# Performance work log

Measured on AMD Instinct MI355X. Metric: run time of the kernel, lower is better.

The kernel has to match this reference:

```python
import jax, jax.numpy as jnp
import numpy as np
import math

B, S, C = 4, 2048, 128
H, DK, DV, K = 8, 64, 64, 3


def setup_inputs() -> dict:
    key = jax.random.key(0)
    ks = jax.random.split(key, 12)
    sd = 0.05
    return {
        "x": jax.random.normal(ks[0], (B, S, C), dtype=jnp.float32),
        "length": jax.random.randint(ks[1], (B,), 1, S + 1, dtype=jnp.int32),
        "wq": jax.random.normal(ks[2], (H * DK, C, K), dtype=jnp.float32) * sd,
        "bq": jnp.zeros((H * DK,), dtype=jnp.float32),
        "wk": jax.random.normal(ks[3], (H * DK, C, K), dtype=jnp.float32) * sd,
        "bk": jnp.zeros((H * DK,), dtype=jnp.float32),
        "wv": jax.random.normal(ks[4], (H * DV, C), dtype=jnp.float32) * sd,
        "bv": jnp.zeros((H * DV,), dtype=jnp.float32),
        "w1": jax.random.normal(ks[5], (DV, H * DV), dtype=jnp.float32) * sd,
        "b1": jnp.zeros((DV,), dtype=jnp.float32),
        "w2": jax.random.normal(ks[6], (1, DV), dtype=jnp.float32) * sd,
        "b2": jnp.zeros((1,), dtype=jnp.float32),
    }


def _causal_conv(x, w, b):
    # x: (b,s,c), w: (o,c,k) torch Conv1d layout -> (b,s,o), causal (left) padding
    y = jax.lax.conv_general_dilated(
        x.transpose(0, 2, 1), w, window_strides=(1,), padding=[(K - 1, 0)],
        dimension_numbers=("NCH", "OIH", "NCH"))
    return y.transpose(0, 2, 1) + b


def _split_heads(x, d):
    b, s, _ = x.shape
    return x.reshape(b, s, H, d).transpose(0, 2, 1, 3)  # (b,h,s,d)


def reference(x, length, wq, bq, wk, bk, wv, bv, w1, b1, w2, b2):
    q = _split_heads(_causal_conv(x, wq, bq), DK)            # (b,h,s,dk)
    k = _split_heads(_causal_conv(x, wk, bk), DK)            # (b,h,s,dk)
    v = _split_heads(jax.nn.relu(x @ wv.T + bv), DV)         # (b,h,s,dv)

    attn = jnp.einsum("bhqd,bhkd->bhqk", q, k) / math.sqrt(DK)
    # future mask: additive -1e9 above the diagonal (matches triu * -1e9 + softmax)
    future = jnp.triu(jnp.ones((S, S), dtype=attn.dtype), k=1) * (-1e9)
    score = jax.nn.softmax(attn + future, axis=-1)
    # padding mask: zero query rows >= length[b]
    row_valid = (jnp.arange(S)[None, :] < length[:, None]).astype(score.dtype)
    score = score * row_valid[:, None, :, None]              # (b,h,s,s)

    out1 = jnp.einsum("bhqk,bhkd->bhqd", score, v)           # (b,h,s,dv)
    out2 = out1.transpose(0, 2, 1, 3).reshape(x.shape[0], S, H * DV)
    out3 = jax.nn.relu(out2 @ w1.T + b1) @ w2.T + b2         # (b,s,1)
    return out3, score
```

## Files before the change

### kernel.cpp

```cpp
#include <hip/hip_runtime.h>

#define S_ 2048
#define C_ 128
#define B_ 4
#define H_ 8
#define D_ 64

typedef __attribute__((ext_vector_type(8))) short bf16x8;
typedef __attribute__((ext_vector_type(4))) float f32x4;

__device__ inline unsigned short f2bf(float f) {
    union { float f; unsigned int u; } c; c.f = f;
    unsigned int u = c.u;
    unsigned int r = (u + 0x7FFFu + ((u >> 16) & 1u)) >> 16;
    return (unsigned short)r;
}
__device__ inline float bf2f(unsigned short s) {
    union { unsigned int u; float f; } c; c.u = ((unsigned int)s) << 16;
    return c.f;
}

__global__ __launch_bounds__(256) void prep_kernel(
    const float* __restrict__ x,
    const float* __restrict__ wq, const float* __restrict__ wk,
    const float* __restrict__ wv, const float* __restrict__ w1,
    unsigned short* __restrict__ xh,
    unsigned short* __restrict__ wPackQ, unsigned short* __restrict__ wPackK,
    unsigned short* __restrict__ wPackV, float* __restrict__ w1T4)
{
    int idx = blockIdx.x * 256 + threadIdx.x;
    if (idx < 262144) {
        float4 v = *(const float4*)&x[idx * 4];
        ushort4 o;
        o.x = f2bf(v.x); o.y = f2bf(v.y); o.z = f2bf(v.z); o.w = f2bf(v.w);
        *(ushort4*)&xh[idx * 4] = o;
    } else if (idx < 458752) {
        int i = idx - 262144;
        int t = i >> 16, r = i & 65535;
        int o = r >> 7, c = r & 127;
        wPackQ[i] = f2bf(wq[o * 384 + c * 3 + t]);
    } else if (idx < 655360) {
        int i = idx - 458752;
        int t = i >> 16, r = i & 65535;
        int o = r >> 7, c = r & 127;
        wPackK[i] = f2bf(wk[o * 384 + c * 3 + t]);
    } else if (idx < 720896) {
        int i = idx - 655360;
        wPackV[i] = f2bf(wv[i]);
    } else if (idx < 753664) {
        int i = idx - 720896;
        int jj = i & 3, d = (i >> 2) & 63, jb = i >> 8;
        w1T4[i] = w1[d * 512 + jb * 4 + jj];
    }
}

__global__ __launch_bounds__(256) void qkv_kernel(
    const unsigned short* __restrict__ xh,
    const unsigned short* __restrict__ wPackQ, const unsigned short* __restrict__ wPackK,
    const unsigned short* __restrict__ wPackV,
    const float* __restrict__ bq, const float* __restrict__ bk,
    const float* __restrict__ bv,
    unsigned short* __restrict__ Qh, unsigned short* __restrict__ Kh,
    unsigned short* __restrict__ VhT)
{
    __shared__ __align__(16) short xs[130 * 136];
    __shared__ __align__(16) short ws[64 * 136];

    int s0 = blockIdx.x * 128;
    int h = blockIdx.y;
    int b = blockIdx.z;
    int bh = b * H_ + h;
    int tid = threadIdx.x;
    int w = tid >> 6;
    int lane = tid & 63;
    int col = lane & 15;
    int quad = lane >> 4;

    for (int i = tid; i < 2080; i += 256) {
        int row = i >> 4, c8 = (i & 15) << 3;
        int s = s0 - 2 + row;
        uint4 v = {0u, 0u, 0u, 0u};
        if (s >= 0) v = *(const uint4*)&xh[((long)b * S_ + s) * C_ + c8];
        *(uint4*)&xs[row * 136 + c8] = v;
    }

    for (int sec = 0; sec < 3; sec++) {
        const unsigned short* wsel = (sec == 0) ? wPackQ : (sec == 1) ? wPackK : wPackV;
        int tlo = (sec == 2) ? 2 : 0;

        f32x4 acc[2][4];
        #pragma unroll
        for (int rt = 0; rt < 2; rt++)
            #pragma unroll
            for (int nt = 0; nt < 4; nt++) acc[rt][nt] = (f32x4){0.f, 0.f, 0.f, 0.f};

        for (int t = tlo; t < 3; t++) {
            if (!(sec == 0 && t == 0)) __syncthreads();
            long wbase = (sec == 2) ? ((long)h * 8192)
                                    : ((long)t * 65536 + (long)h * 8192);
            for (int i = tid; i < 1024; i += 256) {
                int row = i >> 4, c8 = (i & 15) << 3;
                *(uint4*)&ws[row * 136 + c8] = *(const uint4*)&wsel[wbase + row * 128 + c8];
            }
            __syncthreads();

            #pragma unroll
            for (int kc = 0; kc < 4; kc++) {
                int ko = kc * 32 + quad * 8;
                bf16x8 a0 = *(const bf16x8*)&xs[(w * 32 + col + t) * 136 + ko];
                bf16x8 a1 = *(const bf16x8*)&xs[(w * 32 + 16 + col + t) * 136 + ko];
                #pragma unroll
                for (int nt = 0; nt < 4; nt++) {
                    bf16x8 bfr = *(const bf16x8*)&ws[(nt * 16 + col) * 136 + ko];
                    acc[0][nt] = __builtin_amdgcn_mfma_f32_16x16x32_bf16(a0, bfr, acc[0][nt], 0, 0, 0);
                    acc[1][nt] = __builtin_amdgcn_mfma_f32_16x16x32_bf16(a1, bfr, acc[1][nt], 0, 0, 0);
                }
            }
        }

        if (sec == 0) {
            #pragma unroll
            for (int nt = 0; nt < 4; nt++) {
                float bias = bq[h * 64 + nt * 16 + col];
                #pragma unroll
                for (int rt = 0; rt < 2; rt++)
                    #pragma unroll
                    for (int r = 0; r < 4; r++) {
                        int s = s0 + w * 32 + rt * 16 + quad * 4 + r;
                        Qh[((long)bh * S_ + s) * D_ + nt * 16 + col] =
                            f2bf((acc[rt][nt][r] + bias) * 0.18033688011112042f);
                    }
            }
        } else if (sec == 1) {
            #pragma unroll
            for (int nt = 0; nt < 4; nt++) {
                float bias = bk[h * 64 + nt * 16 + col];
                #pragma unroll
                for (int rt = 0; rt < 2; rt++)
                    #pragma unroll
                    for (int r = 0; r < 4; r++) {
                        int s = s0 + w * 32 + rt * 16 + quad * 4 + r;
                        Kh[((long)bh * S_ + s) * D_ + nt * 16 + col] =
                            f2bf(acc[rt][nt][r] + bias);
                    }
            }
        } else {
            __syncthreads();
            #pragma unroll
            for (int nt = 0; nt < 4; nt++) {
                float bias = bv[h * 64 + nt * 16 + col];
                #pragma unroll
                for (int rt = 0; rt < 2; rt++)
                    #pragma unroll
                    for (int r = 0; r < 4; r++) {
                        int sl = w * 32 + rt * 16 + quad * 4 + r;
                        ws[(nt * 16 + col) * 136 + sl] =
                            (short)f2bf(fmaxf(acc[rt][nt][r] + bias, 0.f));
                    }
            }
            __syncthreads();
            for (int i = tid; i < 1024; i += 256) {
                int row = i >> 4, c8 = (i & 15) << 3;
                *(uint4*)&VhT[((long)bh * D_ + row) * S_ + s0 + c8] =
                    *(const uint4*)&ws[row * 136 + c8];
            }
        }
    }
}

#define PST 78
__global__ __launch_bounds__(256) void attn_kernel(
    const unsigned short* __restrict__ Qh, const unsigned short* __restrict__ Kh,
    const unsigned short* __restrict__ VhT, const int* __restrict__ length,
    float* __restrict__ score, float* __restrict__ out2)
{
    __shared__ __align__(16) short Kbuf[2][2][64 * 72];
    __shared__ __align__(16) short Pfh[64 * PST];

    int idx = blockIdx.x;
    int xcd = idx & 7;
    int slot = idx >> 3;
    int t = slot >> 2;
    int qt = (t < 16) ? t : 47 - t;
    int bh = xcd * 4 + (slot & 3);
    int b = bh >> 3, h = bh & 7;
    int q0 = qt * 64;
    int tid = threadIdx.x;
    int w = tid >> 6;
    int lane = tid & 63;
    int col = lane & 15;
    int quad = lane >> 4;
    int len = length[b];

    const unsigned short* Qb = Qh + (long)bh * S_ * D_;
    const unsigned short* Kb = Kh + (long)bh * S_ * D_;
    const unsigned short* Vtb = VhT + (long)bh * D_ * S_;
    float* scb = score + (long)bh * S_ * S_;

    if (q0 >= len) {
        f32x4 z = (f32x4){0.f, 0.f, 0.f, 0.f};
        for (int kt2 = 0; kt2 < 32; kt2++) {
            #pragma unroll
            for (int it = 0; it < 4; it++) {
                int idx2 = tid + it * 256;
                int rr = idx2 >> 4, cc = idx2 & 15;
                __builtin_nontemporal_store(z,
                    (f32x4*)&scb[(long)(q0 + rr) * S_ + kt2 * 64 + cc * 4]);
            }
        }
        #pragma unroll
        for (int it = 0; it < 4; it++) {
            int idx2 = tid + it * 256;
            int rr = idx2 >> 4, cc = idx2 & 15;
            *(f32x4*)&out2[((long)(b * S_ + q0 + rr)) * 512 + h * 64 + cc * 4] = z;
        }
        return;
    }

    int srow_ = tid >> 2, sc16_ = (tid & 3) * 16;

    int arow = w * 16 + col;
    bf16x8 aq0 = *(const bf16x8*)&Qb[(q0 + arow) * D_ + quad * 8];
    bf16x8 aq1 = *(const bf16x8*)&Qb[(q0 + arow) * D_ + 32 + quad * 8];

    float lrun[4];
    #pragma unroll
    for (int r = 0; r < 4; r++) lrun[r] = 0.f;

    {
        *(uint4*)&Kbuf[0][0][srow_ * 72 + sc16_]     = *(const uint4*)&Kb[srow_ * D_ + sc16_];
        *(uint4*)&Kbuf[0][0][srow_ * 72 + sc16_ + 8] = *(const uint4*)&Kb[srow_ * D_ + sc16_ + 8];
    }
    __syncthreads();

    for (int kt = 0; kt <= qt; kt++) {
        int buf = kt & 1;
        if (kt < qt) {
            *(uint4*)&Kbuf[1 - buf][0][srow_ * 72 + sc16_] =
                *(const uint4*)&Kb[((kt + 1) * 64 + srow_) * D_ + sc16_];
            *(uint4*)&Kbuf[1 - buf][0][srow_ * 72 + sc16_ + 8] =
                *(const uint4*)&Kb[((kt + 1) * 64 + srow_) * D_ + sc16_ + 8];
        }

        f32x4 acc[4];
        #pragma unroll
        for (int n = 0; n < 4; n++) acc[n] = (f32x4){0.f, 0.f, 0.f, 0.f};
        #pragma unroll
        for (int n = 0; n < 4; n++) {
            bf16x8 b0 = *(const bf16x8*)&Kbuf[buf][0][(n * 16 + col) * 72 + quad * 8];
            acc[n] = __builtin_amdgcn_mfma_f32_16x16x32_bf16(aq0, b0, acc[n], 0, 0, 0);
            bf16x8 b1 = *(const bf16x8*)&Kbuf[buf][0][(n * 16 + col) * 72 + 32 + quad * 8];
            acc[n] = __builtin_amdgcn_mfma_f32_16x16x32_bf16(aq1, b1, acc[n], 0, 0, 0);
        }
        if (kt == qt) {
            #pragma unroll
            for (int n = 0; n < 4; n++) {
                int kk = kt * 64 + n * 16 + col;
                #pragma unroll
                for (int r = 0; r < 4; r++) {
                    int q = q0 + w * 16 + quad * 4 + r;
                    if (kk > q) acc[n][r] = -1.0e30f;
                }
            }
        }
        #pragma unroll
        for (int r = 0; r < 4; r++) {
            lrun[r] += exp2f(acc[0][r]) + exp2f(acc[1][r]) +
                       exp2f(acc[2][r]) + exp2f(acc[3][r]);
        }
        __syncthreads();
    }

    #pragma unroll
    for (int off = 1; off < 16; off <<= 1) {
        #pragma unroll
        for (int r = 0; r < 4; r++) lrun[r] += __shfl_xor(lrun[r], off, 64);
    }
    float linv[4];
    #pragma unroll
    for (int r = 0; r < 4; r++) linv[r] = 1.0f / lrun[r];

    f32x4 oacc[4];
    #pragma unroll
    for (int n = 0; n < 4; n++) oacc[n] = (f32x4){0.f, 0.f, 0.f, 0.f};

    int prow = w * 16 + quad * 4;
    int rlo = lane >> 4;
    int c4 = (lane & 15) * 4;

#define STAGE2(HALF, KT) do { \
    *(uint4*)&Kbuf[HALF][0][srow_ * 72 + sc16_] = \
        *(const uint4*)&Kb[((KT) * 64 + srow_) * D_ + sc16_]; \
    *(uint4*)&Kbuf[HALF][0][srow_ * 72 + sc16_ + 8] = \
        *(const uint4*)&Kb[((KT) * 64 + srow_) * D_ + sc16_ + 8]; \
    *(uint4*)&Kbuf[HALF][1][srow_ * 72 + sc16_] = \
        *(const uint4*)&Vtb[srow_ * S_ + (KT) * 64 + sc16_]; \
    *(uint4*)&Kbuf[HALF][1][srow_ * 72 + sc16_ + 8] = \
        *(const uint4*)&Vtb[srow_ * S_ + (KT) * 64 + sc16_ + 8]; \
} while (0)

#define TILE2(HALF, KT) do { \
    f32x4 acc[4]; \
    _Pragma("unroll") \
    for (int n = 0; n < 4; n++) acc[n] = (f32x4){0.f, 0.f, 0.f, 0.f}; \
    _Pragma("unroll") \
    for (int n = 0; n < 4; n++) { \
        bf16x8 b0 = *(const bf16x8*)&Kbuf[HALF][0][(n * 16 + col) * 72 + quad * 8]; \
        acc[n] = __builtin_amdgcn_mfma_f32_16x16x32_bf16(aq0, b0, acc[n], 0, 0, 0); \
        bf16x8 b1 = *(const bf16x8*)&Kbuf[HALF][0][(n * 16 + col) * 72 + 32 + quad * 8]; \
        acc[n] = __builtin_amdgcn_mfma_f32_16x16x32_bf16(aq1, b1, acc[n], 0, 0, 0); \
    } \
    bool diag = ((KT) == qt); \
    _Pragma("unroll") \
    for (int n = 0; n < 4; n++) { \
        int kk = (KT) * 64 + n * 16 + col; \
        _Pragma("unroll") \
        for (int r = 0; r < 4; r++) { \
            int q = q0 + prow + r; \
            float pv = exp2f(acc[n][r]) * linv[r]; \
            if (q >= len || (diag && kk > q)) pv = 0.f; \
            Pfh[(prow + r) * PST + n * 16 + col] = (short)f2bf(pv); \
        } \
    } \
    bf16x8 pa0 = *(const bf16x8*)&Pfh[(w * 16 + col) * PST + quad * 8]; \
    bf16x8 pa1 = *(const bf16x8*)&Pfh[(w * 16 + col) * PST + 32 + quad * 8]; \
    _Pragma("unroll") \
    for (int n = 0; n < 4; n++) { \
        bf16x8 vv0 = *(const bf16x8*)&Kbuf[HALF][1][(n * 16 + col) * 72 + quad * 8]; \
        oacc[n] = __builtin_amdgcn_mfma_f32_16x16x32_bf16(pa0, vv0, oacc[n], 0, 0, 0); \
        bf16x8 vv1 = *(const bf16x8*)&Kbuf[HALF][1][(n * 16 + col) * 72 + 32 + quad * 8]; \
        oacc[n] = __builtin_amdgcn_mfma_f32_16x16x32_bf16(pa1, vv1, oacc[n], 0, 0, 0); \
    } \
    _Pragma("unroll") \
    for (int j = 0; j < 4; j++) { \
        int row = w * 16 + j * 4 + rlo; \
        uint2 pk = *(const uint2*)&Pfh[row * PST + c4]; \
        f32x4 v; \
        v[0] = bf2f((unsigned short)(pk.x & 0xFFFFu)); \
        v[1] = bf2f((unsigned short)(pk.x >> 16)); \
        v[2] = bf2f((unsigned short)(pk.y & 0xFFFFu)); \
        v[3] = bf2f((unsigned short)(pk.y >> 16)); \
        __builtin_nontemporal_store(v, \
            (f32x4*)&scb[(long)(q0 + row) * S_ + (KT) * 64 + c4]); \
    } \
} while (0)

    STAGE2(0, 0);
    __syncthreads();
    {
        int kt = 0;
        while (true) {
            if (kt < qt) STAGE2(1, kt + 1);
            TILE2(0, kt);
            __syncthreads();
            kt++; if (kt > qt) break;
            if (kt < qt) STAGE2(0, kt + 1);
            TILE2(1, kt);
            __syncthreads();
            kt++; if (kt > qt) break;
        }
    }
#undef STAGE2
#undef TILE2

    #pragma unroll
    for (int n = 0; n < 4; n++) {
        #pragma unroll
        for (int r = 0; r < 4; r++) {
            int q = q0 + w * 16 + quad * 4 + r;
            out2[((long)(b * S_ + q)) * 512 + h * 64 + n * 16 + col] = oacc[n][r];
        }
    }

    f32x4 z = (f32x4){0.f, 0.f, 0.f, 0.f};
    for (int kt2 = qt + 1; kt2 < 32; kt2++) {
        #pragma unroll
        for (int it = 0; it < 4; it++) {
            int idx2 = tid + it * 256;
            int rr = idx2 >> 4, cc = idx2 & 15;
            __builtin_nontemporal_store(z,
                (f32x4*)&scb[(long)(q0 + rr) * S_ + kt2 * 64 + cc * 4]);
        }
    }
}

__global__ __launch_bounds__(256) void mlp_kernel(
    const float* __restrict__ out2, const float* __restrict__ w1T4,
    const float* __restrict__ b1, const float* __restrict__ w2,
    const float* __restrict__ b2, float* __restrict__ out3)
{
    __shared__ __align__(16) float xr[2048];
    int sg0 = blockIdx.x * 4;
    int tid = threadIdx.x;
    for (int i = tid; i < 512; i += 256)
        *(f32x4*)&xr[i * 4] = *(const f32x4*)&out2[(long)sg0 * 512 + i * 4];
    __syncthreads();

    int sl = tid >> 6, d = tid & 63;
    float acc = 0.f;
    #pragma unroll 4
    for (int jb = 0; jb < 128; jb++) {
        f32x4 xv = *(const f32x4*)&xr[sl * 512 + jb * 4];
        f32x4 wv = *(const f32x4*)&w1T4[jb * 256 + d * 4];
        acc += xv[0] * wv[0] + xv[1] * wv[1] + xv[2] * wv[2] + xv[3] * wv[3];
    }
    float hval = fmaxf(acc + b1[d], 0.f);
    float p = hval * w2[d];
    #pragma unroll
    for (int off = 32; off > 0; off >>= 1) p += __shfl_xor(p, off, 64);
    if (d == 0) out3[sg0 + sl] = p + b2[0];
}

extern "C" void kernel_launch(void* const* d_in, const int* in_sizes, int n_in,
                              void* d_out, int out_size, void* d_ws, size_t ws_size,
                              hipStream_t stream) {
    const float* x      = (const float*)d_in[0];
    const int*   length = (const int*)  d_in[1];
    const float* wq     = (const float*)d_in[2];
    const float* bq     = (const float*)d_in[3];
    const float* wk     = (const float*)d_in[4];
    const float* bk     = (const float*)d_in[5];
    const float* wv     = (const float*)d_in[6];
    const float* bv     = (const float*)d_in[7];
    const float* w1     = (const float*)d_in[8];
    const float* b1     = (const float*)d_in[9];
    const float* w2     = (const float*)d_in[10];
    const float* b2     = (const float*)d_in[11];

    float* out3  = (float*)d_out;
    float* score = (float*)d_out + 8192;

    float* ws  = (float*)d_ws;
    unsigned short* xh     = (unsigned short*)ws;  ws += 524288;
    unsigned short* wPackQ = (unsigned short*)ws;  ws += 98304;
    unsigned short* wPackK = (unsigned short*)ws;  ws += 98304;
    unsigned short* wPackV = (unsigned short*)ws;  ws += 32768;
    float* w1T4 = ws;  ws += 32768;
    unsigned short* Qh  = (unsigned short*)ws;  ws += 2097152;
    unsigned short* Kh  = (unsigned short*)ws;  ws += 2097152;
    unsigned short* VhT = (unsigned short*)ws;  ws += 2097152;
    float* o2  = ws;  ws += 4194304;

    hipLaunchKernelGGL(prep_kernel, dim3(2944), dim3(256), 0, stream,
                       x, wq, wk, wv, w1, xh, wPackQ, wPackK, wPackV, w1T4);
    hipLaunchKernelGGL(qkv_kernel, dim3(16, 8, 4), dim3(256), 0, stream,
                       xh, wPackQ, wPackK, wPackV, bq, bk, bv, Qh, Kh, VhT);
    hipLaunchKernelGGL(attn_kernel, dim3(1024), dim3(256), 0, stream,
                       Qh, Kh, VhT, length, score, o2);
    hipLaunchKernelGGL(mlp_kernel, dim3(2048), dim3(256), 0, stream,
                       o2, w1T4, b1, w2, b2, out3);
}
```

Measured before the change: 634.3 us.

## Split softmax row-sum pass into separate split-K kernel with atomic accumulation

Moves the first pass of the two-pass softmax (row sums of exp scores) out of the attention kernel into a new lsum_kernel. That kernel splits the causal key range into chunks of four tiles across many blocks and combines partial sums with atomicAdd into a buffer zeroed in the prep kernel. The attention kernel then only loads reciprocal sums and runs the second pass. The aim is to remove the serial, load-imbalanced first pass and expose more parallelism. The cost is an extra launch, K reads straight from global memory without LDS staging, and atomic traffic.

```diff
diff --git a/kernel.cpp b/kernel.cpp
--- a/kernel.cpp
+++ b/kernel.cpp
@@ -26,7 +26,8 @@
     const float* __restrict__ wv, const float* __restrict__ w1,
     unsigned short* __restrict__ xh,
     unsigned short* __restrict__ wPackQ, unsigned short* __restrict__ wPackK,
-    unsigned short* __restrict__ wPackV, float* __restrict__ w1T4)
+    unsigned short* __restrict__ wPackV, float* __restrict__ w1T4,
+    float* __restrict__ lbuf)
 {
     int idx = blockIdx.x * 256 + threadIdx.x;
     if (idx < 262144) {
@@ -51,6 +52,8 @@
         int i = idx - 720896;
         int jj = i & 3, d = (i >> 2) & 63, jb = i >> 8;
         w1T4[i] = w1[d * 512 + jb * 4 + jj];
+    } else if (idx < 819200) {
+        lbuf[idx - 753664] = 0.f;
     }
 }
 
@@ -168,10 +171,81 @@
     }
 }
 
+__global__ __launch_bounds__(256) void lsum_kernel(
+    const unsigned short* __restrict__ Qh, const unsigned short* __restrict__ Kh,
+    const int* __restrict__ length, float* __restrict__ lbuf)
+{
+    int qt = blockIdx.x;
+    int bh = blockIdx.y;
+    int ck = blockIdx.z;
+    int kt0 = ck * 4;
+    if (kt0 > qt) return;
+    int b = bh >> 3;
+    int len = length[b];
+    int q0 = qt * 64;
+    if (q0 >= len) return;
+
+    int tid = threadIdx.x;
+    int w = tid >> 6, lane = tid & 63, col = lane & 15, quad = lane >> 4;
+    const unsigned short* Qb = Qh + (long)bh * S_ * D_;
+    const unsigned short* Kb = Kh + (long)bh * S_ * D_;
+
+    int arow = w * 16 + col;
+    bf16x8 aq0 = *(const bf16x8*)&Qb[(q0 + arow) * D_ + quad * 8];
+    bf16x8 aq1 = *(const bf16x8*)&Qb[(q0 + arow) * D_ + 32 + quad * 8];
+
+    float lrun[4];
+    #pragma unroll
+    for (int r = 0; r < 4; r++) lrun[r] = 0.f;
+
+    int ktend = (kt0 + 3 < qt) ? kt0 + 3 : qt;
+    for (int kt = kt0; kt <= ktend; kt++) {
+        f32x4 acc[4];
+        #pragma unroll
+        for (int n = 0; n < 4; n++) acc[n] = (f32x4){0.f, 0.f, 0.f, 0.f};
+        #pragma unroll
+        for (int n = 0; n < 4; n++) {
+            const unsigned short* kp = &Kb[(kt * 64 + n * 16 + col) * D_ + quad * 8];
+            bf16x8 kf0 = *(const bf16x8*)kp;
+            bf16x8 kf1 = *(const bf16x8*)(kp + 32);
+            acc[n] = __builtin_amdgcn_mfma_f32_16x16x32_bf16(aq0, kf0, acc[n], 0, 0, 0);
+            acc[n] = __builtin_amdgcn_mfma_f32_16x16x32_bf16(aq1, kf1, acc[n], 0, 0, 0);
+        }
+        if (kt == qt) {
+            #pragma unroll
+            for (int n = 0; n < 4; n++) {
+                int kk = kt * 64 + n * 16 + col;
+                #pragma unroll
+                for (int r = 0; r < 4; r++) {
+                    int q = q0 + w * 16 + quad * 4 + r;
+                    if (kk > q) acc[n][r] = -1.0e30f;
+                }
+            }
+        }
+        #pragma unroll
+        for (int r = 0; r < 4; r++) {
+            lrun[r] += exp2f(acc[0][r]) + exp2f(acc[1][r]) +
+                       exp2f(acc[2][r]) + exp2f(acc[3][r]);
+        }
+    }
+
+    #pragma unroll
+    for (int off = 1; off < 16; off <<= 1) {
+        #pragma unroll
+        for (int r = 0; r < 4; r++) lrun[r] += __shfl_xor(lrun[r], off, 64);
+    }
+    if (col == 0) {
+        #pragma unroll
+        for (int r = 0; r < 4; r++)
+            atomicAdd(&lbuf[bh * S_ + q0 + w * 16 + quad * 4 + r], lrun[r]);
+    }
+}
+
 #define PST 78
 __global__ __launch_bounds__(256) void attn_kernel(
     const unsigned short* __restrict__ Qh, const unsigned short* __restrict__ Kh,
     const unsigned short* __restrict__ VhT, const int* __restrict__ length,
+    const float* __restrict__ lbuf,
     float* __restrict__ score, float* __restrict__ out2)
 {
     __shared__ __align__(16) short Kbuf[2][2][64 * 72];
@@ -223,62 +297,12 @@
     bf16x8 aq0 = *(const bf16x8*)&Qb[(q0 + arow) * D_ + quad * 8];
     bf16x8 aq1 = *(const bf16x8*)&Qb[(q0 + arow) * D_ + 32 + quad * 8];
 
-    float lrun[4];
-    #pragma unroll
-    for (int r = 0; r < 4; r++) lrun[r] = 0.f;
-
+    float linv[4];
     {
-        *(uint4*)&Kbuf[0][0][srow_ * 72 + sc16_]     = *(const uint4*)&Kb[srow_ * D_ + sc16_];
-        *(uint4*)&Kbuf[0][0][srow_ * 72 + sc16_ + 8] = *(const uint4*)&Kb[srow_ * D_ + sc16_ + 8];
-    }
-    __syncthreads();
-
-    for (int kt = 0; kt <= qt; kt++) {
-        int buf = kt & 1;
-        if (kt < qt) {
-            *(uint4*)&Kbuf[1 - buf][0][srow_ * 72 + sc16_] =
-                *(const uint4*)&Kb[((kt + 1) * 64 + srow_) * D_ + sc16_];
-            *(uint4*)&Kbuf[1 - buf][0][srow_ * 72 + sc16_ + 8] =
-                *(const uint4*)&Kb[((kt + 1) * 64 + srow_) * D_ + sc16_ + 8];
-        }
-
-        f32x4 acc[4];
-        #pragma unroll
-        for (int n = 0; n < 4; n++) acc[n] = (f32x4){0.f, 0.f, 0.f, 0.f};
-        #pragma unroll
-        for (int n = 0; n < 4; n++) {
-            bf16x8 b0 = *(const bf16x8*)&Kbuf[buf][0][(n * 16 + col) * 72 + quad * 8];
-            acc[n] = __builtin_amdgcn_mfma_f32_16x16x32_bf16(aq0, b0, acc[n], 0, 0, 0);
-            bf16x8 b1 = *(const bf16x8*)&Kbuf[buf][0][(n * 16 + col) * 72 + 32 + quad * 8];
-            acc[n] = __builtin_amdgcn_mfma_f32_16x16x32_bf16(aq1, b1, acc[n], 0, 0, 0);
-        }
-        if (kt == qt) {
-            #pragma unroll
-            for (int n = 0; n < 4; n++) {
-                int kk = kt * 64 + n * 16 + col;
-                #pragma unroll
-                for (int r = 0; r < 4; r++) {
-                    int q = q0 + w * 16 + quad * 4 + r;
-                    if (kk > q) acc[n][r] = -1.0e30f;
-                }
-            }
-        }
-        #pragma unroll
-        for (int r = 0; r < 4; r++) {
-            lrun[r] += exp2f(acc[0][r]) + exp2f(acc[1][r]) +
-                       exp2f(acc[2][r]) + exp2f(acc[3][r]);
-        }
-        __syncthreads();
-    }
-
-    #pragma unroll
-    for (int off = 1; off < 16; off <<= 1) {
-        #pragma unroll
-        for (int r = 0; r < 4; r++) lrun[r] += __shfl_xor(lrun[r], off, 64);
-    }
-    float linv[4];
-    #pragma unroll
-    for (int r = 0; r < 4; r++) linv[r] = 1.0f / lrun[r];
+        const float* lb = &lbuf[bh * S_ + q0 + w * 16 + quad * 4];
+        #pragma unroll
+        for (int r = 0; r < 4; r++) linv[r] = 1.0f / lb[r];
+    }
 
     f32x4 oacc[4];
     #pragma unroll
@@ -436,17 +460,20 @@
     unsigned short* wPackK = (unsigned short*)ws;  ws += 98304;
     unsigned short* wPackV = (unsigned short*)ws;  ws += 32768;
     float* w1T4 = ws;  ws += 32768;
+    float* lbuf = ws;  ws += 65536;
     unsigned short* Qh  = (unsigned short*)ws;  ws += 2097152;
     unsigned short* Kh  = (unsigned short*)ws;  ws += 2097152;
     unsigned short* VhT = (unsigned short*)ws;  ws += 2097152;
     float* o2  = ws;  ws += 4194304;
 
-    hipLaunchKernelGGL(prep_kernel, dim3(2944), dim3(256), 0, stream,
-                       x, wq, wk, wv, w1, xh, wPackQ, wPackK, wPackV, w1T4);
+    hipLaunchKernelGGL(prep_kernel, dim3(3200), dim3(256), 0, stream,
+                       x, wq, wk, wv, w1, xh, wPackQ, wPackK, wPackV, w1T4, lbuf);
     hipLaunchKernelGGL(qkv_kernel, dim3(16, 8, 4), dim3(256), 0, stream,
                        xh, wPackQ, wPackK, wPackV, bq, bk, bv, Qh, Kh, VhT);
+    hipLaunchKernelGGL(lsum_kernel, dim3(32, 32, 8), dim3(256), 0, stream,
+                       Qh, Kh, length, lbuf);
     hipLaunchKernelGGL(attn_kernel, dim3(1024), dim3(256), 0, stream,
-                       Qh, Kh, VhT, length, score, o2);
+                       Qh, Kh, VhT, length, lbuf, score, o2);
     hipLaunchKernelGGL(mlp_kernel, dim3(2048), dim3(256), 0, stream,
                        o2, w1T4, b1, w2, b2, out3);
 }
```

New measurement: 675.0 us. 6.4% more time.
